# Kernel tuning notes

Hardware: AMD Instinct MI355X
Metric: run time of the kernel (lower is better)

Reference implementation:

```python
import jax, jax.numpy as jnp
import numpy as np

B, T, C, H = 8, 2048, 1024, 128  # batch, seq (== block_size), embed_size, head_size


def setup_inputs() -> dict:
    key = jax.random.key(0)
    k1, k2, k3, k4 = jax.random.split(key, 4)
    x = jax.random.normal(k1, (B, T, C), dtype=jnp.float32)
    s = 1.0 / np.sqrt(C).astype(np.float32)
    Wq = jax.random.normal(k2, (C, H), dtype=jnp.float32) * s
    Wk = jax.random.normal(k3, (C, H), dtype=jnp.float32) * s
    Wv = jax.random.normal(k4, (C, H), dtype=jnp.float32) * s
    return {"x": x, "Wq": Wq, "Wk": Wk, "Wv": Wv}


def reference(x, Wq, Wk, Wv):
    # x: (B, T, C); projections are bias-free Linears -> x @ W
    Bs, Ts, Cs = x.shape
    q = x @ Wq  # (B, T, H)
    k = x @ Wk  # (B, T, H)
    v = x @ Wv  # (B, T, H)
    # NOTE: original scales by embed_size C ** -0.5, not head_size.
    sims = jnp.einsum('bth,bsh->bts', q, k) * (float(Cs) ** -0.5)  # (B, T, T)
    causal = jnp.tril(jnp.ones((Ts, Ts), dtype=bool))
    sims = jnp.where(causal[None, :, :], sims, -jnp.inf)
    attentions = jax.nn.softmax(sims, axis=-1)  # (B, T, T)
    return attentions @ v  # (B, T, H)
```

## Files before the change

kernel.cpp:

```cpp
#include <hip/hip_runtime.h>


#define B_ 8
#define T_ 2048
#define C_ 1024
#define H_ 128

typedef __attribute__((ext_vector_type(4))) float  f32x4;
typedef __attribute__((ext_vector_type(8))) __bf16 bf16x8;
typedef __attribute__((ext_vector_type(4))) __bf16 bf16x4;
typedef __attribute__((ext_vector_type(4))) short  short4v;

#define QSCALE (0.03125f * 1.44269504088896340736f)

static __device__ __forceinline__ short f2bf(float f) {
  union { __bf16 b; short s; } u;
  u.b = (__bf16)f;
  return u.s;
}

static __device__ __forceinline__ unsigned packbf2(float lo, float hi) {
  union { __bf16 b; unsigned short s; } a, c;
  a.b = (__bf16)lo; c.b = (__bf16)hi;
  return (unsigned)a.s | ((unsigned)c.s << 16);
}

static __device__ __forceinline__ size_t qk_idx(int t, int h, int nk) {
  return ((size_t)((t >> 4) * nk + (h >> 5)) << 9) + (((h >> 3) & 3) << 7)
       + ((t & 15) << 3) + (h & 7);
}
static __device__ __forceinline__ size_t v_idx(int h, int t) {
  return ((size_t)((t >> 4) * 8 + (h >> 4)) << 8) + ((h & 15) << 4) + (t & 15);
}

static __device__ __forceinline__ f32x4 mfma16(unsigned a0, unsigned a1,
                                               unsigned b0, unsigned b1, f32x4 c) {
#if __has_builtin(__builtin_amdgcn_mfma_f32_16x16x16_bf16)
  union { unsigned u[2]; bf16x4 v; } ua, ub;
  ua.u[0] = a0; ua.u[1] = a1; ub.u[0] = b0; ub.u[1] = b1;
  return __builtin_amdgcn_mfma_f32_16x16x16_bf16(ua.v, ub.v, c, 0, 0, 0);
#elif __has_builtin(__builtin_amdgcn_mfma_f32_16x16x16bf16_1k)
  union { unsigned u[2]; short4v v; } ua, ub;
  ua.u[0] = a0; ua.u[1] = a1; ub.u[0] = b0; ub.u[1] = b1;
  return __builtin_amdgcn_mfma_f32_16x16x16bf16_1k(ua.v, ub.v, c, 0, 0, 0);
#else
  union { unsigned u[2]; short4v v; } ua, ub;
  ua.u[0] = a0; ua.u[1] = a1; ub.u[0] = b0; ub.u[1] = b1;
  f32x4 d = c;
  asm volatile("v_mfma_f32_16x16x16_bf16 %0, %1, %2, %0"
               : "+v"(d) : "v"(ua.v), "v"(ub.v));
  return d;
#endif
}

__global__ void prep_wt(const float* __restrict__ Wq, const float* __restrict__ Wk,
                        const float* __restrict__ Wv, short* __restrict__ Wtf) {
  __shared__ float L[64 * 129];
  const int mtx = blockIdx.x >> 4, kc = blockIdx.x & 15;
  const int k0 = kc * 64;
  const float* W = (mtx == 0) ? Wq : (mtx == 1 ? Wk : Wv);
  const float s = (mtx == 0) ? QSCALE : 1.0f;
  for (int i = threadIdx.x; i < 64 * 128; i += 256) {
    int kk = i >> 7, c = i & 127;
    L[kk * 129 + c] = W[(size_t)(k0 + kk) * H_ + c] * s;
  }
  __syncthreads();
  for (int i = threadIdx.x; i < 128 * 64; i += 256) {
    int n = i >> 6, kk = i & 63;
    Wtf[qk_idx(mtx * 128 + n, k0 + kk, 32)] = f2bf(L[kk * 129 + n]);
  }
}

__global__ __launch_bounds__(256) void proj(const float* __restrict__ x,
                                            const short* __restrict__ Wtf,
                                            short* __restrict__ Qf,
                                            short* __restrict__ Kf,
                                            short* __restrict__ Vf) {
  __shared__ __align__(16) short At[2][64 * 128];
  const int tid = threadIdx.x, lane = tid & 63, wv = tid >> 6;
  const int cg = lane & 15, rg = lane >> 4;
  const int lane8 = lane << 3;
  const int g = (blockIdx.x & 7) * 64 + (blockIdx.x >> 3);
  const int mb = g >> 1, bn = g & 1;
  const int m0 = mb * 64;
  const int nfrag0 = bn * 12 + wv * 3;
  const float* xblk = x + (size_t)m0 * C_;

  f32x4 acc[4][3];
#pragma unroll
  for (int i = 0; i < 4; ++i)
#pragma unroll
    for (int j = 0; j < 3; ++j) {
      f32x4 z = {0.f, 0.f, 0.f, 0.f};
      acc[i][j] = z;
    }

  f32x4 ldr[4][2];

#define PLOAD(kt)                                                              \
  { _Pragma("unroll") for (int it = 0; it < 4; ++it) {                         \
      int ls = it * 256 + tid; int r = ls >> 4, sc = ls & 15;                  \
      const float* p = xblk + (size_t)r * C_ + (kt) * 128 + sc * 8;            \
      ldr[it][0] = *(const f32x4*)p; ldr[it][1] = *(const f32x4*)(p + 4);      \
  } }

#define PWRITE(bf)                                                             \
  { _Pragma("unroll") for (int it = 0; it < 4; ++it) {                         \
      int ls = it * 256 + tid; int r = ls >> 4, sc = ls & 15;                  \
      bf16x8 tv;                                                               \
      tv[0] = (__bf16)ldr[it][0][0]; tv[1] = (__bf16)ldr[it][0][1];            \
      tv[2] = (__bf16)ldr[it][0][2]; tv[3] = (__bf16)ldr[it][0][3];            \
      tv[4] = (__bf16)ldr[it][1][0]; tv[5] = (__bf16)ldr[it][1][1];            \
      tv[6] = (__bf16)ldr[it][1][2]; tv[7] = (__bf16)ldr[it][1][3];            \
      *(bf16x8*)&At[bf][r * 128 + ((sc ^ (r & 7)) << 3)] = tv;                 \
  } }

  PLOAD(0);
  PWRITE(0);
  __syncthreads();

  for (int kt = 0; kt < 8; ++kt) {
    const int cur = kt & 1;
    if (kt < 7) PLOAD(kt + 1);

#pragma unroll
    for (int ks = 0; ks < 4; ++ks) {
      bf16x8 af[4];
#pragma unroll
      for (int fm = 0; fm < 4; ++fm) {
        int r = fm * 16 + cg;
        int slot = (ks * 4 + rg) ^ (r & 7);
        af[fm] = *(const bf16x8*)&At[cur][r * 128 + (slot << 3)];
      }
#pragma unroll
      for (int nf = 0; nf < 3; ++nf) {
        bf16x8 bfr = *(const bf16x8*)&Wtf[((size_t)((nfrag0 + nf) * 32 + kt * 4 + ks) << 9) + lane8];
#pragma unroll
        for (int fm = 0; fm < 4; ++fm)
          acc[fm][nf] = __builtin_amdgcn_mfma_f32_16x16x32_bf16(af[fm], bfr, acc[fm][nf], 0, 0, 0);
      }
    }
    if (kt < 7) PWRITE(cur ^ 1);
    __syncthreads();
  }
#undef PLOAD
#undef PWRITE

#pragma unroll
  for (int fm = 0; fm < 4; ++fm) {
#pragma unroll
    for (int nf = 0; nf < 3; ++nf) {
      int n = (nfrag0 + nf) * 16 + cg;
      int rowm = m0 + fm * 16 + rg * 4;
      size_t boff = (size_t)(rowm >> 11) << 18;
      f32x4 v = acc[fm][nf];
      if (n < 128) {
#pragma unroll
        for (int r = 0; r < 4; ++r)
          Qf[boff + qk_idx((rowm + r) & 2047, n, 4)] = f2bf(v[r]);
      } else if (n < 256) {
#pragma unroll
        for (int r = 0; r < 4; ++r)
          Kf[boff + qk_idx((rowm + r) & 2047, n - 128, 4)] = f2bf(v[r]);
      } else {
#pragma unroll
        for (int r = 0; r < 4; ++r)
          Vf[boff + v_idx(n - 256, (rowm + r) & 2047)] = f2bf(v[r]);
      }
    }
  }
}

#define OCW 132
__global__ __launch_bounds__(512) void attn(const short* __restrict__ Qf,
                                            const short* __restrict__ Kf,
                                            const short* __restrict__ Vf,
                                            float* __restrict__ out) {
  __shared__ __align__(16) float OC[4][32 * OCW];
  __shared__ float Mml[8][32], Lml[8][32];
  const int tid = threadIdx.x, lane = tid & 63, wv = tid >> 6;
  const int cg = lane & 15, rg = lane >> 4;
  const int lane8 = lane << 3;
  const int bid = blockIdx.x;
  const int b = bid & 7;
  const int p = bid >> 3;
  const int grp = wv >> 2;
  const int wvl = wv & 3;
  const int qg = grp ? p : (63 - p);
  const int q0 = qg << 5;
  const int NT = (q0 + 95) >> 6;
  const int SPW = (NT + 3) >> 2;
  const int t0 = wvl * SPW;
  const int t1 = (t0 + SPW < NT) ? (t0 + SPW) : NT;

  const short* Qp = Qf + ((size_t)b << 18);
  const short* Kp = Kf + ((size_t)b << 18);
  const short* Vp = Vf + ((size_t)b << 18);
  const float NEG_INF = -__builtin_inff();

  bf16x8 qf[2][4];
#pragma unroll
  for (int qc = 0; qc < 2; ++qc)
#pragma unroll
    for (int ks = 0; ks < 4; ++ks)
      qf[qc][ks] = *(const bf16x8*)&Qp[((size_t)(((q0 >> 4) + qc) * 4 + ks) << 9) + lane8];

  f32x4 o[8][2];
#pragma unroll
  for (int f = 0; f < 8; ++f)
#pragma unroll
    for (int qc = 0; qc < 2; ++qc) { f32x4 z = {0.f, 0.f, 0.f, 0.f}; o[f][qc] = z; }
  float m[2] = {NEG_INF, NEG_INF}, lsum[2] = {0.0f, 0.0f};

  bf16x8 kf[4][4];
#define LOADK(t_)                                                              \
  { const short* ktp = Kp + (size_t)(t_) * 8192;                               \
    _Pragma("unroll") for (int nf_ = 0; nf_ < 4; ++nf_)                        \
    _Pragma("unroll") for (int ks_ = 0; ks_ < 4; ++ks_)                        \
      kf[nf_][ks_] = *(const bf16x8*)&ktp[((nf_ * 4 + ks_) << 9) + lane8]; }

  if (t0 < t1) LOADK(t0);

  for (int t = t0; t < t1; ++t) {
    const int kv0 = t * 64;
    const short* vtile = Vp + (size_t)t * 8192;

    f32x4 s[4][2];
#pragma unroll
    for (int nf = 0; nf < 4; ++nf)
#pragma unroll
      for (int qc = 0; qc < 2; ++qc) { f32x4 z = {0.f, 0.f, 0.f, 0.f}; s[nf][qc] = z; }

    __builtin_amdgcn_s_setprio(1);
#pragma unroll
    for (int nf = 0; nf < 4; ++nf)
#pragma unroll
      for (int ks = 0; ks < 4; ++ks) {
        s[nf][0] = __builtin_amdgcn_mfma_f32_16x16x32_bf16(kf[nf][ks], qf[0][ks], s[nf][0], 0, 0, 0);
        s[nf][1] = __builtin_amdgcn_mfma_f32_16x16x32_bf16(kf[nf][ks], qf[1][ks], s[nf][1], 0, 0, 0);
      }
    __builtin_amdgcn_s_setprio(0);

    if (t + 1 < t1) LOADK(t + 1);

    unsigned v0a[8], v0b[8];
#pragma unroll
    for (int hf = 0; hf < 8; ++hf) {
      const unsigned* vp = (const unsigned*)&vtile[(hf << 8) + (cg << 4) + (rg << 2)];
      v0a[hf] = vp[0]; v0b[hf] = vp[1];
    }

    if (t == NT - 1) {
#pragma unroll
      for (int nf = 0; nf < 4; ++nf)
#pragma unroll
        for (int qc = 0; qc < 2; ++qc)
#pragma unroll
          for (int r = 0; r < 4; ++r)
            if (kv0 + nf * 16 + rg * 4 + r > q0 + qc * 16 + cg) s[nf][qc][r] = NEG_INF;
    }

    unsigned pk[4][2][2];
#pragma unroll
    for (int qc = 0; qc < 2; ++qc) {
      float pm = s[0][qc][0];
#pragma unroll
      for (int nf = 0; nf < 4; ++nf)
#pragma unroll
        for (int r = 0; r < 4; ++r) pm = fmaxf(pm, s[nf][qc][r]);
      pm = fmaxf(pm, __shfl_xor(pm, 16));
      pm = fmaxf(pm, __shfl_xor(pm, 32));
      if (!__all(pm <= m[qc] + 8.0f)) {
        float mn = fmaxf(m[qc], pm);
        float sf = exp2f(m[qc] - mn);
        m[qc] = mn;
        lsum[qc] *= sf;
#pragma unroll
        for (int f = 0; f < 8; ++f)
#pragma unroll
          for (int r = 0; r < 4; ++r) o[f][qc][r] *= sf;
      }
      float mq = m[qc];
#pragma unroll
      for (int nf = 0; nf < 4; ++nf) {
        float p0 = exp2f(s[nf][qc][0] - mq), p1 = exp2f(s[nf][qc][1] - mq);
        float p2 = exp2f(s[nf][qc][2] - mq), p3 = exp2f(s[nf][qc][3] - mq);
        lsum[qc] += (p0 + p1) + (p2 + p3);
        pk[nf][qc][0] = packbf2(p0, p1);
        pk[nf][qc][1] = packbf2(p2, p3);
      }
    }

    __builtin_amdgcn_s_setprio(1);
#pragma unroll
    for (int hf = 0; hf < 8; ++hf) {
      o[hf][0] = mfma16(v0a[hf], v0b[hf], pk[0][0][0], pk[0][0][1], o[hf][0]);
      o[hf][1] = mfma16(v0a[hf], v0b[hf], pk[0][1][0], pk[0][1][1], o[hf][1]);
    }
#pragma unroll
    for (int nf = 1; nf < 4; ++nf) {
      const unsigned b00 = pk[nf][0][0], b01 = pk[nf][0][1];
      const unsigned b10 = pk[nf][1][0], b11 = pk[nf][1][1];
#pragma unroll
      for (int hf = 0; hf < 8; ++hf) {
        const unsigned* vp = (const unsigned*)&vtile[((nf * 8 + hf) << 8) + (cg << 4) + (rg << 2)];
        unsigned v0 = vp[0], v1 = vp[1];
        o[hf][0] = mfma16(v0, v1, b00, b01, o[hf][0]);
        o[hf][1] = mfma16(v0, v1, b10, b11, o[hf][1]);
      }
    }
    __builtin_amdgcn_s_setprio(0);
  }
#undef LOADK

#pragma unroll
  for (int qc = 0; qc < 2; ++qc) {
    lsum[qc] += __shfl_xor(lsum[qc], 16);
    lsum[qc] += __shfl_xor(lsum[qc], 32);
  }
  if (lane < 16) {
#pragma unroll
    for (int qc = 0; qc < 2; ++qc) {
      Mml[wv][qc * 16 + lane] = m[qc];
      Lml[wv][qc * 16 + lane] = lsum[qc];
    }
  }
  if (grp == 0) {
#pragma unroll
    for (int hf = 0; hf < 8; ++hf)
#pragma unroll
      for (int qc = 0; qc < 2; ++qc)
        *(f32x4*)&OC[wv][(qc * 16 + cg) * OCW + hf * 16 + rg * 4] = o[hf][qc];
  }
  __syncthreads();
  {
    const int qb = (63 - p) << 5;
    for (int i = tid; i < 32 * 128; i += 512) {
      int row = i >> 7, col = i & 127;
      float ms = fmaxf(fmaxf(Mml[0][row], Mml[1][row]), fmaxf(Mml[2][row], Mml[3][row]));
      float accv = 0.f, lacc = 0.f;
#pragma unroll
      for (int w = 0; w < 4; ++w) {
        float sc = exp2f(Mml[w][row] - ms);
        lacc += sc * Lml[w][row];
        accv += sc * OC[w][row * OCW + col];
      }
      out[(size_t)(b * T_ + qb + row) * H_ + col] = accv / lacc;
    }
  }
  __syncthreads();
  if (grp == 1) {
#pragma unroll
    for (int hf = 0; hf < 8; ++hf)
#pragma unroll
      for (int qc = 0; qc < 2; ++qc)
        *(f32x4*)&OC[wvl][(qc * 16 + cg) * OCW + hf * 16 + rg * 4] = o[hf][qc];
  }
  __syncthreads();
  {
    const int qb = p << 5;
    for (int i = tid; i < 32 * 128; i += 512) {
      int row = i >> 7, col = i & 127;
      float ms = fmaxf(fmaxf(Mml[4][row], Mml[5][row]), fmaxf(Mml[6][row], Mml[7][row]));
      float accv = 0.f, lacc = 0.f;
#pragma unroll
      for (int w = 0; w < 4; ++w) {
        float sc = exp2f(Mml[4 + w][row] - ms);
        lacc += sc * Lml[4 + w][row];
        accv += sc * OC[w][row * OCW + col];
      }
      out[(size_t)(b * T_ + qb + row) * H_ + col] = accv / lacc;
    }
  }
}

extern "C" void kernel_launch(void* const* d_in, const int* in_sizes, int n_in,
                              void* d_out, int out_size, void* d_ws, size_t ws_size,
                              hipStream_t stream) {
  const float* x  = (const float*)d_in[0];
  const float* Wq = (const float*)d_in[1];
  const float* Wk = (const float*)d_in[2];
  const float* Wv = (const float*)d_in[3];
  float* out = (float*)d_out;
  char* ws = (char*)d_ws;

  short* Wtf = (short*)(ws);
  short* Qf  = (short*)(ws + ((size_t)1 << 20));
  short* Kf  = (short*)(ws + ((size_t)5 << 20));
  short* Vf  = (short*)(ws + ((size_t)9 << 20));

  prep_wt<<<dim3(48), dim3(256), 0, stream>>>(Wq, Wk, Wv, Wtf);
  proj<<<dim3(512), dim3(256), 0, stream>>>(x, Wtf, Qf, Kf, Vf);
  attn<<<dim3(256), dim3(512), 0, stream>>>(Qf, Kf, Vf, out);
}
```

Before: 69.30 us.

## Split projection N across four blocks and prefetch weight fragments in registers

The projection kernel now launches 1024 blocks, each covering 96 output columns instead of 192. Inside a block the four waves form a 2x2 grid over rows and columns, so each wave holds fewer accumulators. The weight fragments are double-buffered in registers and loaded one k-step ahead to hide global latency. The cost is that each x tile is loaded and converted twice as often, which doubles x traffic from global memory.

New measurement: 75.55 us. 9.0% more time.

```diff
diff --git a/kernel.cpp b/kernel.cpp
--- a/kernel.cpp
+++ b/kernel.cpp
@@ -80,15 +80,16 @@
   const int tid = threadIdx.x, lane = tid & 63, wv = tid >> 6;
   const int cg = lane & 15, rg = lane >> 4;
   const int lane8 = lane << 3;
-  const int g = (blockIdx.x & 7) * 64 + (blockIdx.x >> 3);
-  const int mb = g >> 1, bn = g & 1;
+  const int mh = wv >> 1, ng = wv & 1;
+  const int g = (blockIdx.x & 7) * 128 + (blockIdx.x >> 3);
+  const int mb = g >> 2, bn = g & 3;
   const int m0 = mb * 64;
-  const int nfrag0 = bn * 12 + wv * 3;
+  const int nfrag0 = bn * 6 + ng * 3;
   const float* xblk = x + (size_t)m0 * C_;
 
-  f32x4 acc[4][3];
-#pragma unroll
-  for (int i = 0; i < 4; ++i)
+  f32x4 acc[2][3];
+#pragma unroll
+  for (int i = 0; i < 2; ++i)
 #pragma unroll
     for (int j = 0; j < 3; ++j) {
       f32x4 z = {0.f, 0.f, 0.f, 0.f};
@@ -115,43 +116,56 @@
       *(bf16x8*)&At[bf][r * 128 + ((sc ^ (r & 7)) << 3)] = tv;                 \
   } }
 
+#define LOADB(dst, kt, ks)                                                     \
+  { _Pragma("unroll") for (int nf = 0; nf < 3; ++nf)                           \
+      dst[nf] = *(const bf16x8*)&Wtf[((size_t)((nfrag0 + nf) * 32 + (kt) * 4 + (ks)) << 9) + lane8]; }
+
+#define KSTEP(cur, ks, bb)                                                     \
+  { bf16x8 af[2];                                                              \
+    _Pragma("unroll") for (int fm = 0; fm < 2; ++fm) {                         \
+      int r = mh * 32 + fm * 16 + cg;                                          \
+      int slot = ((ks) * 4 + rg) ^ (r & 7);                                    \
+      af[fm] = *(const bf16x8*)&At[cur][r * 128 + (slot << 3)];                \
+    }                                                                          \
+    _Pragma("unroll") for (int nf = 0; nf < 3; ++nf) {                         \
+      acc[0][nf] = __builtin_amdgcn_mfma_f32_16x16x32_bf16(af[0], bb[nf], acc[0][nf], 0, 0, 0); \
+      acc[1][nf] = __builtin_amdgcn_mfma_f32_16x16x32_bf16(af[1], bb[nf], acc[1][nf], 0, 0, 0); \
+    } }
+
   PLOAD(0);
   PWRITE(0);
+  bf16x8 b0[3], b1[3];
+  LOADB(b0, 0, 0);
+  LOADB(b1, 0, 1);
   __syncthreads();
 
   for (int kt = 0; kt < 8; ++kt) {
     const int cur = kt & 1;
     if (kt < 7) PLOAD(kt + 1);
 
-#pragma unroll
-    for (int ks = 0; ks < 4; ++ks) {
-      bf16x8 af[4];
-#pragma unroll
-      for (int fm = 0; fm < 4; ++fm) {
-        int r = fm * 16 + cg;
-        int slot = (ks * 4 + rg) ^ (r & 7);
-        af[fm] = *(const bf16x8*)&At[cur][r * 128 + (slot << 3)];
-      }
-#pragma unroll
-      for (int nf = 0; nf < 3; ++nf) {
-        bf16x8 bfr = *(const bf16x8*)&Wtf[((size_t)((nfrag0 + nf) * 32 + kt * 4 + ks) << 9) + lane8];
-#pragma unroll
-        for (int fm = 0; fm < 4; ++fm)
-          acc[fm][nf] = __builtin_amdgcn_mfma_f32_16x16x32_bf16(af[fm], bfr, acc[fm][nf], 0, 0, 0);
-      }
-    }
+    KSTEP(cur, 0, b0);
+    LOADB(b0, kt, 2);
+    KSTEP(cur, 1, b1);
+    LOADB(b1, kt, 3);
+    KSTEP(cur, 2, b0);
+    if (kt < 7) LOADB(b0, kt + 1, 0);
+    KSTEP(cur, 3, b1);
+    if (kt < 7) LOADB(b1, kt + 1, 1);
+
     if (kt < 7) PWRITE(cur ^ 1);
     __syncthreads();
   }
 #undef PLOAD
 #undef PWRITE
-
-#pragma unroll
-  for (int fm = 0; fm < 4; ++fm) {
+#undef LOADB
+#undef KSTEP
+
+#pragma unroll
+  for (int fm = 0; fm < 2; ++fm) {
 #pragma unroll
     for (int nf = 0; nf < 3; ++nf) {
       int n = (nfrag0 + nf) * 16 + cg;
-      int rowm = m0 + fm * 16 + rg * 4;
+      int rowm = m0 + mh * 32 + fm * 16 + rg * 4;
       size_t boff = (size_t)(rowm >> 11) << 18;
       f32x4 v = acc[fm][nf];
       if (n < 128) {
@@ -390,6 +404,6 @@
   short* Vf  = (short*)(ws + ((size_t)9 << 20));
 
   prep_wt<<<dim3(48), dim3(256), 0, stream>>>(Wq, Wk, Wv, Wtf);
-  proj<<<dim3(512), dim3(256), 0, stream>>>(x, Wtf, Qf, Kf, Vf);
+  proj<<<dim3(1024), dim3(256), 0, stream>>>(x, Wtf, Qf, Kf, Vf);
   attn<<<dim3(256), dim3(512), 0, stream>>>(Qf, Kf, Vf, out);
 }
```

## Split projection K dimension across two wave groups with LDS reduction

Applied to the files above, without the earlier changes.

The projection kernel now runs 512 threads per block. Two groups of four waves each handle half of the C=1024 reduction dimension, with a separate double-buffered LDS tile per group. Partial accumulators from the second group are reduced through LDS before the first group writes Q/K/V. This halves the serial K-loop length per wave and adds memory-level parallelism. In exchange it doubles LDS use per block and adds a reduction step plus an extra barrier, which may lower the number of blocks resident per CU.

Result: slower. 73.43 us (+6.0%).

```diff
diff --git a/kernel.cpp b/kernel.cpp
--- a/kernel.cpp
+++ b/kernel.cpp
@@ -71,20 +71,22 @@
   }
 }
 
-__global__ __launch_bounds__(256) void proj(const float* __restrict__ x,
+__global__ __launch_bounds__(512) void proj(const float* __restrict__ x,
                                             const short* __restrict__ Wtf,
                                             short* __restrict__ Qf,
                                             short* __restrict__ Kf,
                                             short* __restrict__ Vf) {
-  __shared__ __align__(16) short At[2][64 * 128];
+  __shared__ __align__(16) short At[2][2][64 * 128];
   const int tid = threadIdx.x, lane = tid & 63, wv = tid >> 6;
   const int cg = lane & 15, rg = lane >> 4;
   const int lane8 = lane << 3;
+  const int kh = wv >> 2, ng = wv & 3;
+  const int tidh = tid & 255;
   const int g = (blockIdx.x & 7) * 64 + (blockIdx.x >> 3);
   const int mb = g >> 1, bn = g & 1;
   const int m0 = mb * 64;
-  const int nfrag0 = bn * 12 + wv * 3;
-  const float* xblk = x + (size_t)m0 * C_;
+  const int nfrag0 = bn * 12 + ng * 3;
+  const float* xblk = x + (size_t)m0 * C_ + kh * 512;
 
   f32x4 acc[4][3];
 #pragma unroll
@@ -99,29 +101,29 @@
 
 #define PLOAD(kt)                                                              \
   { _Pragma("unroll") for (int it = 0; it < 4; ++it) {                         \
-      int ls = it * 256 + tid; int r = ls >> 4, sc = ls & 15;                  \
+      int ls = it * 256 + tidh; int r = ls >> 4, sc = ls & 15;                 \
       const float* p = xblk + (size_t)r * C_ + (kt) * 128 + sc * 8;            \
       ldr[it][0] = *(const f32x4*)p; ldr[it][1] = *(const f32x4*)(p + 4);      \
   } }
 
 #define PWRITE(bf)                                                             \
   { _Pragma("unroll") for (int it = 0; it < 4; ++it) {                         \
-      int ls = it * 256 + tid; int r = ls >> 4, sc = ls & 15;                  \
+      int ls = it * 256 + tidh; int r = ls >> 4, sc = ls & 15;                 \
       bf16x8 tv;                                                               \
       tv[0] = (__bf16)ldr[it][0][0]; tv[1] = (__bf16)ldr[it][0][1];            \
       tv[2] = (__bf16)ldr[it][0][2]; tv[3] = (__bf16)ldr[it][0][3];            \
       tv[4] = (__bf16)ldr[it][1][0]; tv[5] = (__bf16)ldr[it][1][1];            \
       tv[6] = (__bf16)ldr[it][1][2]; tv[7] = (__bf16)ldr[it][1][3];            \
-      *(bf16x8*)&At[bf][r * 128 + ((sc ^ (r & 7)) << 3)] = tv;                 \
+      *(bf16x8*)&At[kh][bf][r * 128 + ((sc ^ (r & 7)) << 3)] = tv;             \
   } }
 
   PLOAD(0);
   PWRITE(0);
   __syncthreads();
 
-  for (int kt = 0; kt < 8; ++kt) {
+  for (int kt = 0; kt < 4; ++kt) {
     const int cur = kt & 1;
-    if (kt < 7) PLOAD(kt + 1);
+    if (kt < 3) PLOAD(kt + 1);
 
 #pragma unroll
     for (int ks = 0; ks < 4; ++ks) {
@@ -130,21 +132,44 @@
       for (int fm = 0; fm < 4; ++fm) {
         int r = fm * 16 + cg;
         int slot = (ks * 4 + rg) ^ (r & 7);
-        af[fm] = *(const bf16x8*)&At[cur][r * 128 + (slot << 3)];
+        af[fm] = *(const bf16x8*)&At[kh][cur][r * 128 + (slot << 3)];
       }
 #pragma unroll
       for (int nf = 0; nf < 3; ++nf) {
-        bf16x8 bfr = *(const bf16x8*)&Wtf[((size_t)((nfrag0 + nf) * 32 + kt * 4 + ks) << 9) + lane8];
+        int kslice = kh * 16 + kt * 4 + ks;
+        bf16x8 bfr = *(const bf16x8*)&Wtf[((size_t)((nfrag0 + nf) * 32 + kslice) << 9) + lane8];
 #pragma unroll
         for (int fm = 0; fm < 4; ++fm)
           acc[fm][nf] = __builtin_amdgcn_mfma_f32_16x16x32_bf16(af[fm], bfr, acc[fm][nf], 0, 0, 0);
       }
     }
-    if (kt < 7) PWRITE(cur ^ 1);
+    if (kt < 3) PWRITE(cur ^ 1);
     __syncthreads();
   }
 #undef PLOAD
 #undef PWRITE
+
+  {
+    float* Red = (float*)&At[0][0][0];
+    float* myR = Red + ng * 3072;
+    if (kh == 1) {
+#pragma unroll
+      for (int fm = 0; fm < 4; ++fm)
+#pragma unroll
+        for (int nf = 0; nf < 3; ++nf)
+          *(f32x4*)&myR[(((fm * 3 + nf) << 6) + lane) << 2] = acc[fm][nf];
+    }
+    __syncthreads();
+    if (kh == 1) return;
+#pragma unroll
+    for (int fm = 0; fm < 4; ++fm)
+#pragma unroll
+      for (int nf = 0; nf < 3; ++nf) {
+        f32x4 p = *(const f32x4*)&myR[(((fm * 3 + nf) << 6) + lane) << 2];
+#pragma unroll
+        for (int r = 0; r < 4; ++r) acc[fm][nf][r] += p[r];
+      }
+  }
 
 #pragma unroll
   for (int fm = 0; fm < 4; ++fm) {
@@ -390,6 +415,6 @@
   short* Vf  = (short*)(ws + ((size_t)9 << 20));
 
   prep_wt<<<dim3(48), dim3(256), 0, stream>>>(Wq, Wk, Wv, Wtf);
-  proj<<<dim3(512), dim3(256), 0, stream>>>(x, Wtf, Qf, Kf, Vf);
+  proj<<<dim3(512), dim3(512), 0, stream>>>(x, Wtf, Qf, Kf, Vf);
   attn<<<dim3(256), dim3(512), 0, stream>>>(Qf, Kf, Vf, out);
 }
```
